# Performance work log

Hardware: AMD Instinct MI355X
Metric: run time of the kernel (lower is better)

## Reference

```python
import jax, jax.numpy as jnp
import numpy as np

NUM_ITER = 20
EPS = 1e-8


def _conv(x, w, pad):
    # x: [N, Cin, H, W], w: [Cout, Cin, kh, kw] (cross-correlation, like torch conv2d)
    return jax.lax.conv_general_dilated(
        x, w, window_strides=(1, 1), padding=pad,
        dimension_numbers=('NCHW', 'OIHW', 'NCHW'))


def setup_inputs() -> dict:
    key = jax.random.key(0)
    x = jax.random.normal(key, (2, 4, 3, 256, 256), dtype=jnp.float32)
    return {
        'x': x,
        'lam': jnp.array([0.02], dtype=jnp.float32),
        'tau': jnp.array([0.25], dtype=jnp.float32),
        'theta': jnp.array([0.1], dtype=jnp.float32),
        'wx': jnp.array([[-1.0, 1.0, 0.0]], dtype=jnp.float32),
        'wy': jnp.array([[-1.0], [1.0], [0.0]], dtype=jnp.float32),
    }


def reference(x, lam, tau, theta, wx, wy):
    # x: [2, B, C, H, W] -> pairs of single-channel images [NB, 2, H, W]
    F, B, C, H, W = x.shape
    NB = B * C
    xx = jnp.moveaxis(x.reshape(2, NB, H, W), 0, 1)  # [NB, 2, H, W]

    dt = x.dtype
    gx = jnp.array([[-1., 0., 1.], [-2., 0., 2.], [-1., 0., 1.]], dt) / 6.0
    gy = jnp.array([[-1., -2., -1.], [0., 0., 0.], [1., 2., 1.]], dt) / 6.0
    grad_w = jnp.stack([gx, gy])[:, None]          # [2,1,3,3] image gradient (fixed)
    gxu = jnp.array([[0., 0., 0.], [0., -1., 1.], [0., 0., 0.]], dt)
    gyu = jnp.array([[0., 0., 0.], [0., -1., 0.], [0., 1., 0.]], dt)
    grad_u_w = jnp.stack([gxu, gyu])[:, None]      # [2,1,3,3] flow gradient (fixed)
    wx_k = wx[None, None]                          # [1,1,1,3] trainable divergence stencil
    wy_k = wy[None, None]                          # [1,1,3,1]

    rho_c = (xx[:, 1] - xx[:, 0])[:, None]                       # [NB,1,H,W]
    grad_im = _conv(xx[:, 1:], grad_w, [(1, 1), (1, 1)])         # [NB,2,H,W]
    norm_grad = jnp.sum(grad_im * grad_im, axis=1, keepdims=True) + EPS

    u = jnp.zeros((NB, 2, H, W), dt)
    p1 = jnp.zeros((NB, 2, H, W), dt)
    p2 = jnp.zeros((NB, 2, H, W), dt)

    tl = theta * lam       # [1]
    tt = tau / theta       # [1]

    def div(p):  # p: [NB,2,H,W] -> [NB,1,H,W]
        return (_conv(p[:, 0:1], wx_k, [(0, 0), (1, 1)]) +
                _conv(p[:, 1:2], wy_k, [(1, 1), (0, 0)]))

    def body(carry, _):
        u, p1, p2 = carry
        rho = rho_c + jnp.sum(grad_im * u, axis=1, keepdims=True)
        th = tl * norm_grad
        v = u - jnp.where(jnp.abs(rho) < th,
                          rho * grad_im / norm_grad,
                          tl * grad_im * jnp.sign(rho))
        u0 = v[:, 0] + theta * div(p1)[:, 0]
        u1 = v[:, 1] + theta * div(p2)[:, 0]
        u = jnp.stack([u0, u1], axis=1)
        g1 = _conv(u[:, 0:1], grad_u_w, [(1, 1), (1, 1)])
        g2 = _conv(u[:, 1:2], grad_u_w, [(1, 1), (1, 1)])
        p1 = (p1 + tt * g1) / (1.0 + tt * jnp.sum(jnp.abs(g1), axis=1, keepdims=True))
        p2 = (p2 + tt * g2) / (1.0 + tt * jnp.sum(jnp.abs(g2), axis=1, keepdims=True))
        return (u, p1, p2), None

    (u, p1, p2), _ = jax.lax.scan(body, (u, p1, p2), None, length=NUM_ITER)
    return u.reshape(B, C, 2, H, W)
```

## Files before the change

kernel.cpp:

```cpp
#include <hip/hip_runtime.h>

#define W 256
#define H 256
#define HW (W*H)
#define NB 12
#define ROWS 16
#define BPI (H/ROWS)
#define NBLK (NB*BPI)
#define NTHREADS 1024
#define NUM_ITER 20
#define TVEPS 1e-8f
#define HPLANES 8
#define FLAG_MAGIC 0x5A170000


__device__ __forceinline__ float aload(const float* p) {
    return __hip_atomic_load(p, __ATOMIC_RELAXED, __HIP_MEMORY_SCOPE_AGENT);
}
__device__ __forceinline__ void astore(float* p, float v) {
    __hip_atomic_store(p, v, __ATOMIC_RELAXED, __HIP_MEMORY_SCOPE_AGENT);
}
__device__ __forceinline__ void waitflag(const int* f, int tgt) {
    while (__hip_atomic_load(f, __ATOMIC_RELAXED, __HIP_MEMORY_SCOPE_AGENT) != tgt)
        __builtin_amdgcn_s_sleep(1);
    asm volatile("" ::: "memory");
}
__device__ __forceinline__ void setflag(int* f, int tgt) {
    asm volatile("s_waitcnt vmcnt(0)" ::: "memory");
    __hip_atomic_store(f, tgt, __ATOMIC_RELAXED, __HIP_MEMORY_SCOPE_AGENT);
}

#define LD4(dst, ptr) { const float4 _t = *reinterpret_cast<const float4*>(ptr); \
                        dst[0]=_t.x; dst[1]=_t.y; dst[2]=_t.z; dst[3]=_t.w; }
#define ST4(ptr, src) { float4 _t; _t.x=src[0]; _t.y=src[1]; _t.z=src[2]; _t.w=src[3]; \
                        *reinterpret_cast<float4*>(ptr) = _t; }

__global__ __launch_bounds__(NTHREADS, 1) void tvl1_wave_kernel(
    const float* __restrict__ xin,
    const float* __restrict__ lam,
    const float* __restrict__ tau,
    const float* __restrict__ theta,
    const float* __restrict__ wxv,
    const float* __restrict__ wyv,
    float* __restrict__ uout,
    float* __restrict__ halo,
    int* __restrict__ flags)
{
    __shared__ float xu0[ROWS+1][W];
    __shared__ float xu1[ROWS+1][W];
    __shared__ float xq1[ROWS][W];
    __shared__ float xq2[ROWS][W];
    __shared__ float s_g16[3][W];

    const int tid  = threadIdx.x;
    const int lane = tid & 63;
    const int wv   = tid >> 6;
    const int x0   = lane << 2;
    const int b    = blockIdx.x;
    const int n    = b / BPI, bi = b % BPI;
    const int r0   = bi * ROWS;
    const int grow = r0 + wv;
    const bool notTop = (bi > 0), notBot = (bi < BPI-1);

    const float th0 = theta[0];
    const float tl  = th0 * lam[0];
    const float tt  = tau[0] / th0;
    const float wx0 = wxv[0], wx1 = wxv[1], wx2 = wxv[2];
    const float wy0 = wyv[0], wy1 = wyv[1], wy2 = wyv[2];

    const float* __restrict__ I0 = xin + (size_t)n * HW;
    const float* __restrict__ I1 = xin + (size_t)(NB + n) * HW;

    float rho[4], gxr[4], gyr[4];
    auto grad4 = [&](int row, float* rr, float* ggx, float* ggy) {
        #pragma unroll
        for (int c = 0; c < 4; ++c) {
            const int xc = x0 + c;
            const int idx = row * W + xc;
            const bool xm = xc > 0, xp = xc < W-1, ym = row > 0, yp = row < H-1;
            float a00=0.f,a01=0.f,a02=0.f,a10=0.f,a12=0.f,a20=0.f,a21=0.f,a22=0.f;
            if (ym) { a01=I1[idx-W]; if (xm) a00=I1[idx-W-1]; if (xp) a02=I1[idx-W+1]; }
            if (xm) a10=I1[idx-1];
            if (xp) a12=I1[idx+1];
            if (yp) { a21=I1[idx+W]; if (xm) a20=I1[idx+W-1]; if (xp) a22=I1[idx+W+1]; }
            ggx[c] = ((a02-a00) + 2.f*(a12-a10) + (a22-a20)) * (1.f/6.f);
            ggy[c] = ((a20-a00) + 2.f*(a21-a01) + (a22-a02)) * (1.f/6.f);
            rr[c]  = I1[idx] - I0[idx];
        }
    };
    grad4(grow, rho, gxr, gyr);
    if (wv == 14 && notBot) {
        float r2[4], g2x[4], g2y[4];
        grad4(r0 + ROWS, r2, g2x, g2y);
        ST4(&s_g16[0][x0], r2); ST4(&s_g16[1][x0], g2x); ST4(&s_g16[2][x0], g2y);
    }

    for (int k = tid; k < (ROWS+1)*W; k += NTHREADS) { (&xu0[0][0])[k]=0.f; (&xu1[0][0])[k]=0.f; }
    for (int k = tid; k < ROWS*W;     k += NTHREADS) { (&xq1[0][0])[k]=0.f; (&xq2[0][0])[k]=0.f; }
    float u0[4]={0,0,0,0}, u1[4]={0,0,0,0};
    float p1x[4]={0,0,0,0}, p1y[4]={0,0,0,0}, p2x[4]={0,0,0,0}, p2y[4]={0,0,0,0};
    __syncthreads();

    auto ustep4 = [&](const float* rr, const float* ggx, const float* ggy,
                      const float* uu0, const float* uu1,
                      const float* x1m, const float* x1c, const float* x1p,
                      const float* q1m, const float* q1c, const float* q1p,
                      const float* x2m, const float* x2c, const float* x2p,
                      const float* q2m, const float* q2c, const float* q2p,
                      float* o0, float* o1) {
        #pragma unroll
        for (int c = 0; c < 4; ++c) {
            const float r  = rr[c] + ggx[c]*uu0[c] + ggy[c]*uu1[c];
            const float ng = ggx[c]*ggx[c] + ggy[c]*ggy[c] + TVEPS;
            const float th = tl * ng;
            const float sg = (r > 0.f) ? 1.f : ((r < 0.f) ? -1.f : 0.f);
            const float f  = (fabsf(r) < th) ? (r / ng) : (tl * sg);
            const float d1 = wx0*x1m[c] + wx1*x1c[c] + wx2*x1p[c]
                           + wy0*q1m[c] + wy1*q1c[c] + wy2*q1p[c];
            const float d2 = wx0*x2m[c] + wx1*x2c[c] + wx2*x2p[c]
                           + wy0*q2m[c] + wy1*q2c[c] + wy2*q2p[c];
            o0[c] = (uu0[c] - f*ggx[c]) + th0*d1;
            o1[c] = (uu1[c] - f*ggy[c]) + th0*d2;
        }
    };

    for (int it = 0; it < NUM_ITER; ++it) {
        const bool last = (it == NUM_ITER-1);

        float hym1[4]={0,0,0,0}, hym2[4]={0,0,0,0};
        float hyp1[4]={0,0,0,0}, hyp2[4]={0,0,0,0};
        float c16x1[4]={0,0,0,0}, c16x2[4]={0,0,0,0};
        float c16c1[4]={0,0,0,0}, c16c2[4]={0,0,0,0};
        float c16p1[4]={0,0,0,0}, c16p2[4]={0,0,0,0};

        if (it > 0) {
            const float* hb = halo + (size_t)(it-1) * NBLK * HPLANES * W;
            int* fb = flags + (size_t)(it-1) * 3 * NBLK;
            const int tgt = FLAG_MAGIC | (it-1);
            if (wv == 0 && notTop) {
                if (lane == 0) waitflag(&fb[2*NBLK + (b-1)], tgt);
                const float* hu = hb + (size_t)(b-1) * HPLANES * W;
                #pragma unroll
                for (int c = 0; c < 4; ++c) {
                    hym1[c] = aload(hu + 6*W + x0 + c);
                    hym2[c] = aload(hu + 7*W + x0 + c);
                }
            }
            if (wv == 15 && notBot) {
                if (lane == 0) waitflag(&fb[0*NBLK + (b+1)], tgt);
                const float* hd = hb + (size_t)(b+1) * HPLANES * W;
                #pragma unroll
                for (int c = 0; c < 4; ++c) {
                    hyp1[c] = aload(hd + 1*W + x0 + c);
                    hyp2[c] = aload(hd + 3*W + x0 + c);
                }
            }
            if (wv == 14 && notBot && !last) {
                if (lane < 2) waitflag(&fb[lane*NBLK + (b+1)], tgt);
                const float* hd = hb + (size_t)(b+1) * HPLANES * W;
                #pragma unroll
                for (int c = 0; c < 4; ++c) {
                    c16x1[c] = aload(hd + 0*W + x0 + c);
                    c16c1[c] = aload(hd + 1*W + x0 + c);
                    c16x2[c] = aload(hd + 2*W + x0 + c);
                    c16c2[c] = aload(hd + 3*W + x0 + c);
                    c16p1[c] = aload(hd + 4*W + x0 + c);
                    c16p2[c] = aload(hd + 5*W + x0 + c);
                }
            }
        }

        float pym1[4], pym2[4], pyp1[4], pyp2[4];
        if (wv > 0) { LD4(pym1, &xq1[wv-1][x0]); LD4(pym2, &xq2[wv-1][x0]); }
        else        { for (int c=0;c<4;++c){ pym1[c]=hym1[c]; pym2[c]=hym2[c]; } }
        if (wv < ROWS-1) { LD4(pyp1, &xq1[wv+1][x0]); LD4(pyp2, &xq2[wv+1][x0]); }
        else             { for (int c=0;c<4;++c){ pyp1[c]=hyp1[c]; pyp2[c]=hyp2[c]; } }

        float l1 = __shfl_up(p1x[3], 1);   float l2 = __shfl_up(p2x[3], 1);
        if (lane == 0) { l1 = 0.f; l2 = 0.f; }
        float r1 = __shfl_down(p1x[0], 1); float r2 = __shfl_down(p2x[0], 1);
        if (lane == 63) { r1 = 0.f; r2 = 0.f; }
        const float p1xm[4] = { l1, p1x[0], p1x[1], p1x[2] };
        const float p1xp[4] = { p1x[1], p1x[2], p1x[3], r1 };
        const float p2xm[4] = { l2, p2x[0], p2x[1], p2x[2] };
        const float p2xp[4] = { p2x[1], p2x[2], p2x[3], r2 };

        float nu0[4], nu1[4];
        ustep4(rho, gxr, gyr, u0, u1,
               p1xm, p1x, p1xp, pym1, p1y, pyp1,
               p2xm, p2x, p2xp, pym2, p2y, pyp2, nu0, nu1);
        #pragma unroll
        for (int c = 0; c < 4; ++c) { u0[c] = nu0[c]; u1[c] = nu1[c]; }

        if (last) {
            float* __restrict__ o0 = uout + (size_t)(2*n)   * HW + (size_t)grow * W + x0;
            float* __restrict__ o1 = uout + (size_t)(2*n+1) * HW + (size_t)grow * W + x0;
            ST4(o0, u0); ST4(o1, u1);
            break;
        }

        ST4(&xu0[wv][x0], u0); ST4(&xu1[wv][x0], u1);

        if (wv == 14 && notBot) {
            float g16r[4], g16x[4], g16y[4], q115[4], q215[4], u160[4], u161[4];
            LD4(g16r, &s_g16[0][x0]); LD4(g16x, &s_g16[1][x0]); LD4(g16y, &s_g16[2][x0]);
            LD4(q115, &xq1[ROWS-1][x0]); LD4(q215, &xq2[ROWS-1][x0]);
            LD4(u160, &xu0[ROWS][x0]);   LD4(u161, &xu1[ROWS][x0]);
            float hl1 = __shfl_up(c16x1[3], 1), hl2 = __shfl_up(c16x2[3], 1);
            if (lane == 0) { hl1 = 0.f; hl2 = 0.f; }
            float hr1 = __shfl_down(c16x1[0], 1), hr2 = __shfl_down(c16x2[0], 1);
            if (lane == 63) { hr1 = 0.f; hr2 = 0.f; }
            const float h1m[4] = { hl1, c16x1[0], c16x1[1], c16x1[2] };
            const float h1p[4] = { c16x1[1], c16x1[2], c16x1[3], hr1 };
            const float h2m[4] = { hl2, c16x2[0], c16x2[1], c16x2[2] };
            const float h2p[4] = { c16x2[1], c16x2[2], c16x2[3], hr2 };
            float n160[4], n161[4];
            ustep4(g16r, g16x, g16y, u160, u161,
                   h1m, c16x1, h1p, q115, c16c1, c16p1,
                   h2m, c16x2, h2p, q215, c16c2, c16p2, n160, n161);
            ST4(&xu0[ROWS][x0], n160); ST4(&xu1[ROWS][x0], n161);
        }
        __syncthreads();

        float uy0[4], uy1[4];
        const bool lastRow = (grow == H-1);
        if (!lastRow) { LD4(uy0, &xu0[wv+1][x0]); LD4(uy1, &xu1[wv+1][x0]); }
        else          { for (int c=0;c<4;++c){ uy0[c]=0.f; uy1[c]=0.f; } }
        float ur0 = __shfl_down(u0[0], 1), ur1 = __shfl_down(u1[0], 1);
        if (lane == 63) { ur0 = 0.f; ur1 = 0.f; }
        #pragma unroll
        for (int c = 0; c < 4; ++c) {
            const float uxp0 = (c < 3) ? u0[c+1] : ur0;
            const float uxp1 = (c < 3) ? u1[c+1] : ur1;
            const float g1x = uxp0 - u0[c];
            const float g1y = uy0[c] - u0[c];
            const float g2x = uxp1 - u1[c];
            const float g2y = uy1[c] - u1[c];
            const float den1 = 1.f + tt * (fabsf(g1x) + fabsf(g1y));
            const float den2 = 1.f + tt * (fabsf(g2x) + fabsf(g2y));
            p1x[c] = (p1x[c] + tt*g1x) / den1;
            p1y[c] = (p1y[c] + tt*g1y) / den1;
            p2x[c] = (p2x[c] + tt*g2x) / den2;
            p2y[c] = (p2y[c] + tt*g2y) / den2;
        }
        ST4(&xq1[wv][x0], p1y); ST4(&xq2[wv][x0], p2y);

        float* hwp = halo + ((size_t)it * NBLK + b) * HPLANES * W;
        int* fw = flags + (size_t)it * 3 * NBLK;
        const int ftgt = FLAG_MAGIC | it;
        if (wv == 0) {
            #pragma unroll
            for (int c = 0; c < 4; ++c) {
                astore(hwp + 0*W + x0 + c, p1x[c]);
                astore(hwp + 1*W + x0 + c, p1y[c]);
                astore(hwp + 2*W + x0 + c, p2x[c]);
                astore(hwp + 3*W + x0 + c, p2y[c]);
            }
            if (lane == 0) setflag(&fw[0*NBLK + b], ftgt);
        } else if (wv == 1) {
            #pragma unroll
            for (int c = 0; c < 4; ++c) {
                astore(hwp + 4*W + x0 + c, p1y[c]);
                astore(hwp + 5*W + x0 + c, p2y[c]);
            }
            if (lane == 0) setflag(&fw[1*NBLK + b], ftgt);
        } else if (wv == ROWS-1) {
            #pragma unroll
            for (int c = 0; c < 4; ++c) {
                astore(hwp + 6*W + x0 + c, p1y[c]);
                astore(hwp + 7*W + x0 + c, p2y[c]);
            }
            if (lane == 0) setflag(&fw[2*NBLK + b], ftgt);
        }
        __syncthreads();
    }
}


__global__ void precompute_kernel(const float* __restrict__ x,
                                  float* __restrict__ u,
                                  float* __restrict__ ws) {
    const int row = blockIdx.x;
    const int n = row / H, y = row % H;
    const int xx = threadIdx.x;
    const int idx = y * W + xx;
    const float* __restrict__ I0 = x + (size_t)n * HW;
    const float* __restrict__ I1 = x + (size_t)(NB + n) * HW;
    float* __restrict__ p1  = ws;
    float* __restrict__ p2  = ws + (size_t)2 * NB * HW;
    float* __restrict__ rho = ws + (size_t)4 * NB * HW;
    float* __restrict__ gxp = ws + (size_t)5 * NB * HW;
    float* __restrict__ gyp = ws + (size_t)6 * NB * HW;
    const float i1c = I1[idx];
    const bool xm = xx > 0, xp = xx < W - 1, ym = y > 0, yp = y < H - 1;
    float a00=0.f,a01=0.f,a02=0.f,a10=0.f,a12=0.f,a20=0.f,a21=0.f,a22=0.f;
    if (ym) { a01 = I1[idx-W]; if (xm) a00 = I1[idx-W-1]; if (xp) a02 = I1[idx-W+1]; }
    if (xm) a10 = I1[idx-1];
    if (xp) a12 = I1[idx+1];
    if (yp) { a21 = I1[idx+W]; if (xm) a20 = I1[idx+W-1]; if (xp) a22 = I1[idx+W+1]; }
    const float gxv = ((a02-a00) + 2.f*(a12-a10) + (a22-a20)) * (1.f/6.f);
    const float gyv = ((a20-a00) + 2.f*(a21-a01) + (a22-a02)) * (1.f/6.f);
    const size_t np = (size_t)n * HW;
    rho[np+idx] = i1c - I0[idx];
    gxp[np+idx] = gxv;
    gyp[np+idx] = gyv;
    u[(size_t)(2*n)*HW + idx] = 0.f;   u[(size_t)(2*n+1)*HW + idx] = 0.f;
    p1[(size_t)(2*n)*HW + idx] = 0.f;  p1[(size_t)(2*n+1)*HW + idx] = 0.f;
    p2[(size_t)(2*n)*HW + idx] = 0.f;  p2[(size_t)(2*n+1)*HW + idx] = 0.f;
}

__global__ void u_kernel(const float* __restrict__ ws,
                         float* __restrict__ u,
                         const float* __restrict__ lam,
                         const float* __restrict__ theta,
                         const float* __restrict__ wxv,
                         const float* __restrict__ wyv) {
    const int row = blockIdx.x;
    const int n = row / H, y = row % H;
    const int xx = threadIdx.x;
    const int idx = y * W + xx;
    const size_t np = (size_t)n * HW;
    const float* __restrict__ p1  = ws;
    const float* __restrict__ p2  = ws + (size_t)2 * NB * HW;
    const float* __restrict__ rho_c = ws + (size_t)4 * NB * HW;
    const float* __restrict__ gxp = ws + (size_t)5 * NB * HW;
    const float* __restrict__ gyp = ws + (size_t)6 * NB * HW;
    const float th0 = theta[0];
    const float tl = th0 * lam[0];
    const float wx0 = wxv[0], wx1 = wxv[1], wx2 = wxv[2];
    const float wy0 = wyv[0], wy1 = wyv[1], wy2 = wyv[2];
    const float gx = gxp[np+idx];
    const float gy = gyp[np+idx];
    float* __restrict__ u0p = u + (size_t)(2*n)*HW;
    float* __restrict__ u1p = u + (size_t)(2*n+1)*HW;
    const float u0 = u0p[idx], u1 = u1p[idx];
    const float rho = rho_c[np+idx] + gx*u0 + gy*u1;
    const float ng = gx*gx + gy*gy + TVEPS;
    const float th = tl * ng;
    float s0, s1;
    if (fabsf(rho) < th) { const float d = rho/ng; s0 = d*gx; s1 = d*gy; }
    else { const float sg = (rho > 0.f) ? 1.f : ((rho < 0.f) ? -1.f : 0.f);
           s0 = tl*gx*sg; s1 = tl*gy*sg; }
    const float v0 = u0 - s0, v1 = u1 - s1;
    const float* __restrict__ p1x = p1 + (size_t)(2*n)*HW;
    const float* __restrict__ p1y = p1 + (size_t)(2*n+1)*HW;
    const float* __restrict__ p2x = p2 + (size_t)(2*n)*HW;
    const float* __restrict__ p2y = p2 + (size_t)(2*n+1)*HW;
    float d1 = wx1*p1x[idx] + wy1*p1y[idx];
    float d2 = wx1*p2x[idx] + wy1*p2y[idx];
    if (xx > 0)     { d1 += wx0*p1x[idx-1]; d2 += wx0*p2x[idx-1]; }
    if (xx < W-1)   { d1 += wx2*p1x[idx+1]; d2 += wx2*p2x[idx+1]; }
    if (y > 0)      { d1 += wy0*p1y[idx-W]; d2 += wy0*p2y[idx-W]; }
    if (y < H-1)    { d1 += wy2*p1y[idx+W]; d2 += wy2*p2y[idx+W]; }
    u0p[idx] = v0 + th0*d1;
    u1p[idx] = v1 + th0*d2;
}

__global__ void p_kernel(const float* __restrict__ u,
                         float* __restrict__ ws,
                         const float* __restrict__ tau,
                         const float* __restrict__ theta) {
    const int row = blockIdx.x;
    const int n = row / H, y = row % H;
    const int xx = threadIdx.x;
    const int idx = y * W + xx;
    float* __restrict__ p1 = ws;
    float* __restrict__ p2 = ws + (size_t)2 * NB * HW;
    const float tt = tau[0] / theta[0];
    const float* __restrict__ u0p = u + (size_t)(2*n)*HW;
    const float* __restrict__ u1p = u + (size_t)(2*n+1)*HW;
    const float c0 = u0p[idx];
    const float g1x = ((xx < W-1) ? u0p[idx+1] : 0.f) - c0;
    const float g1y = ((y < H-1) ? u0p[idx+W] : 0.f) - c0;
    const float c1 = u1p[idx];
    const float g2x = ((xx < W-1) ? u1p[idx+1] : 0.f) - c1;
    const float g2y = ((y < H-1) ? u1p[idx+W] : 0.f) - c1;
    float* __restrict__ p1x = p1 + (size_t)(2*n)*HW;
    float* __restrict__ p1y = p1 + (size_t)(2*n+1)*HW;
    float* __restrict__ p2x = p2 + (size_t)(2*n)*HW;
    float* __restrict__ p2y = p2 + (size_t)(2*n+1)*HW;
    const float den1 = 1.f + tt * (fabsf(g1x) + fabsf(g1y));
    p1x[idx] = (p1x[idx] + tt*g1x) / den1;
    p1y[idx] = (p1y[idx] + tt*g1y) / den1;
    const float den2 = 1.f + tt * (fabsf(g2x) + fabsf(g2y));
    p2x[idx] = (p2x[idx] + tt*g2x) / den2;
    p2y[idx] = (p2y[idx] + tt*g2y) / den2;
}

extern "C" void kernel_launch(void* const* d_in, const int* in_sizes, int n_in,
                              void* d_out, int out_size, void* d_ws, size_t ws_size,
                              hipStream_t stream) {
    const float* x     = (const float*)d_in[0];
    const float* lam   = (const float*)d_in[1];
    const float* tau   = (const float*)d_in[2];
    const float* theta = (const float*)d_in[3];
    const float* wxv   = (const float*)d_in[4];
    const float* wyv   = (const float*)d_in[5];
    float* u = (float*)d_out;

    const size_t halo_floats = (size_t)(NUM_ITER-1) * NBLK * HPLANES * W;
    const size_t need = halo_floats * sizeof(float)
                      + (size_t)(NUM_ITER-1) * 3 * NBLK * sizeof(int);

    if (ws_size >= need) {
        float* halo = (float*)d_ws;
        int* flags = (int*)((char*)d_ws + halo_floats * sizeof(float));
        void* args[] = { (void*)&x, (void*)&lam, (void*)&tau, (void*)&theta,
                         (void*)&wxv, (void*)&wyv, (void*)&u, (void*)&halo, (void*)&flags };
        hipLaunchCooperativeKernel((void*)tvl1_wave_kernel, dim3(NBLK), dim3(NTHREADS),
                                   args, 0, stream);
    } else {
        float* ws = (float*)d_ws;
        const dim3 grid(NB * H);
        const dim3 block(W);
        precompute_kernel<<<grid, block, 0, stream>>>(x, u, ws);
        for (int it = 0; it < NUM_ITER; ++it) {
            u_kernel<<<grid, block, 0, stream>>>(ws, u, lam, theta, wxv, wyv);
            p_kernel<<<grid, block, 0, stream>>>(u, ws, tau, theta);
        }
    }
}
```

Measured before the change: 126.8 us.

## Exchange boundary u row via halo instead of redundant row-16 recompute

Replaces the redundant recomputation of the next block's first u row, which needed six halo planes of p state, with a mid-iteration exchange: each block publishes its top u row and the bottom wave waits on the neighbour's flag before the p step. The halo shrinks from 8 to 6 planes, and extra shared-memory rows and setup work are dropped. Divisions are also replaced with hardware reciprocal approximations. The cost is an extra inter-block dependency wait inside each iteration, which can add latency on the critical path, and approximate reciprocals slightly change numerics.

```diff
diff --git a/kernel.cpp b/kernel.cpp
--- a/kernel.cpp
+++ b/kernel.cpp
@@ -10,7 +10,7 @@
 #define NTHREADS 1024
 #define NUM_ITER 20
 #define TVEPS 1e-8f
-#define HPLANES 8
+#define HPLANES 6
 #define FLAG_MAGIC 0x5A170000
 
 
@@ -29,13 +29,14 @@
     asm volatile("s_waitcnt vmcnt(0)" ::: "memory");
     __hip_atomic_store(f, tgt, __ATOMIC_RELAXED, __HIP_MEMORY_SCOPE_AGENT);
 }
+__device__ __forceinline__ float fastrcp(float x) { return __builtin_amdgcn_rcpf(x); }
 
 #define LD4(dst, ptr) { const float4 _t = *reinterpret_cast<const float4*>(ptr); \
                         dst[0]=_t.x; dst[1]=_t.y; dst[2]=_t.z; dst[3]=_t.w; }
 #define ST4(ptr, src) { float4 _t; _t.x=src[0]; _t.y=src[1]; _t.z=src[2]; _t.w=src[3]; \
                         *reinterpret_cast<float4*>(ptr) = _t; }
 
-__global__ __launch_bounds__(NTHREADS, 1) void tvl1_wave_kernel(
+__global__ __launch_bounds__(NTHREADS, 1) void tvl1_uex_kernel(
     const float* __restrict__ xin,
     const float* __restrict__ lam,
     const float* __restrict__ tau,
@@ -46,11 +47,10 @@
     float* __restrict__ halo,
     int* __restrict__ flags)
 {
-    __shared__ float xu0[ROWS+1][W];
-    __shared__ float xu1[ROWS+1][W];
+    __shared__ float xu0[ROWS][W];
+    __shared__ float xu1[ROWS][W];
     __shared__ float xq1[ROWS][W];
     __shared__ float xq2[ROWS][W];
-    __shared__ float s_g16[3][W];
 
     const int tid  = threadIdx.x;
     const int lane = tid & 63;
@@ -72,100 +72,55 @@
     const float* __restrict__ I1 = xin + (size_t)(NB + n) * HW;
 
     float rho[4], gxr[4], gyr[4];
-    auto grad4 = [&](int row, float* rr, float* ggx, float* ggy) {
+    {
         #pragma unroll
         for (int c = 0; c < 4; ++c) {
             const int xc = x0 + c;
-            const int idx = row * W + xc;
-            const bool xm = xc > 0, xp = xc < W-1, ym = row > 0, yp = row < H-1;
+            const int idx = grow * W + xc;
+            const bool xm = xc > 0, xp = xc < W-1, ym = grow > 0, yp = grow < H-1;
             float a00=0.f,a01=0.f,a02=0.f,a10=0.f,a12=0.f,a20=0.f,a21=0.f,a22=0.f;
             if (ym) { a01=I1[idx-W]; if (xm) a00=I1[idx-W-1]; if (xp) a02=I1[idx-W+1]; }
             if (xm) a10=I1[idx-1];
             if (xp) a12=I1[idx+1];
             if (yp) { a21=I1[idx+W]; if (xm) a20=I1[idx+W-1]; if (xp) a22=I1[idx+W+1]; }
-            ggx[c] = ((a02-a00) + 2.f*(a12-a10) + (a22-a20)) * (1.f/6.f);
-            ggy[c] = ((a20-a00) + 2.f*(a21-a01) + (a22-a02)) * (1.f/6.f);
-            rr[c]  = I1[idx] - I0[idx];
-        }
-    };
-    grad4(grow, rho, gxr, gyr);
-    if (wv == 14 && notBot) {
-        float r2[4], g2x[4], g2y[4];
-        grad4(r0 + ROWS, r2, g2x, g2y);
-        ST4(&s_g16[0][x0], r2); ST4(&s_g16[1][x0], g2x); ST4(&s_g16[2][x0], g2y);
+            gxr[c] = ((a02-a00) + 2.f*(a12-a10) + (a22-a20)) * (1.f/6.f);
+            gyr[c] = ((a20-a00) + 2.f*(a21-a01) + (a22-a02)) * (1.f/6.f);
+            rho[c] = I1[idx] - I0[idx];
+        }
     }
 
-    for (int k = tid; k < (ROWS+1)*W; k += NTHREADS) { (&xu0[0][0])[k]=0.f; (&xu1[0][0])[k]=0.f; }
-    for (int k = tid; k < ROWS*W;     k += NTHREADS) { (&xq1[0][0])[k]=0.f; (&xq2[0][0])[k]=0.f; }
+    for (int k = tid; k < ROWS*W; k += NTHREADS) {
+        (&xu0[0][0])[k]=0.f; (&xu1[0][0])[k]=0.f;
+        (&xq1[0][0])[k]=0.f; (&xq2[0][0])[k]=0.f;
+    }
     float u0[4]={0,0,0,0}, u1[4]={0,0,0,0};
     float p1x[4]={0,0,0,0}, p1y[4]={0,0,0,0}, p2x[4]={0,0,0,0}, p2y[4]={0,0,0,0};
     __syncthreads();
 
-    auto ustep4 = [&](const float* rr, const float* ggx, const float* ggy,
-                      const float* uu0, const float* uu1,
-                      const float* x1m, const float* x1c, const float* x1p,
-                      const float* q1m, const float* q1c, const float* q1p,
-                      const float* x2m, const float* x2c, const float* x2p,
-                      const float* q2m, const float* q2c, const float* q2p,
-                      float* o0, float* o1) {
-        #pragma unroll
-        for (int c = 0; c < 4; ++c) {
-            const float r  = rr[c] + ggx[c]*uu0[c] + ggy[c]*uu1[c];
-            const float ng = ggx[c]*ggx[c] + ggy[c]*ggy[c] + TVEPS;
-            const float th = tl * ng;
-            const float sg = (r > 0.f) ? 1.f : ((r < 0.f) ? -1.f : 0.f);
-            const float f  = (fabsf(r) < th) ? (r / ng) : (tl * sg);
-            const float d1 = wx0*x1m[c] + wx1*x1c[c] + wx2*x1p[c]
-                           + wy0*q1m[c] + wy1*q1c[c] + wy2*q1p[c];
-            const float d2 = wx0*x2m[c] + wx1*x2c[c] + wx2*x2p[c]
-                           + wy0*q2m[c] + wy1*q2c[c] + wy2*q2p[c];
-            o0[c] = (uu0[c] - f*ggx[c]) + th0*d1;
-            o1[c] = (uu1[c] - f*ggy[c]) + th0*d2;
-        }
-    };
-
     for (int it = 0; it < NUM_ITER; ++it) {
         const bool last = (it == NUM_ITER-1);
 
         float hym1[4]={0,0,0,0}, hym2[4]={0,0,0,0};
         float hyp1[4]={0,0,0,0}, hyp2[4]={0,0,0,0};
-        float c16x1[4]={0,0,0,0}, c16x2[4]={0,0,0,0};
-        float c16c1[4]={0,0,0,0}, c16c2[4]={0,0,0,0};
-        float c16p1[4]={0,0,0,0}, c16p2[4]={0,0,0,0};
-
         if (it > 0) {
-            const float* hb = halo + (size_t)(it-1) * NBLK * HPLANES * W;
             int* fb = flags + (size_t)(it-1) * 3 * NBLK;
             const int tgt = FLAG_MAGIC | (it-1);
             if (wv == 0 && notTop) {
-                if (lane == 0) waitflag(&fb[2*NBLK + (b-1)], tgt);
-                const float* hu = hb + (size_t)(b-1) * HPLANES * W;
+                if (lane == 0) waitflag(&fb[1*NBLK + (b-1)], tgt);
+                const float* hu = halo + ((size_t)(it-1)*NBLK + (b-1)) * HPLANES * W;
                 #pragma unroll
                 for (int c = 0; c < 4; ++c) {
-                    hym1[c] = aload(hu + 6*W + x0 + c);
-                    hym2[c] = aload(hu + 7*W + x0 + c);
+                    hym1[c] = aload(hu + 2*W + x0 + c);
+                    hym2[c] = aload(hu + 3*W + x0 + c);
                 }
             }
             if (wv == 15 && notBot) {
                 if (lane == 0) waitflag(&fb[0*NBLK + (b+1)], tgt);
-                const float* hd = hb + (size_t)(b+1) * HPLANES * W;
+                const float* hd = halo + ((size_t)(it-1)*NBLK + (b+1)) * HPLANES * W;
                 #pragma unroll
                 for (int c = 0; c < 4; ++c) {
-                    hyp1[c] = aload(hd + 1*W + x0 + c);
-                    hyp2[c] = aload(hd + 3*W + x0 + c);
-                }
-            }
-            if (wv == 14 && notBot && !last) {
-                if (lane < 2) waitflag(&fb[lane*NBLK + (b+1)], tgt);
-                const float* hd = hb + (size_t)(b+1) * HPLANES * W;
-                #pragma unroll
-                for (int c = 0; c < 4; ++c) {
-                    c16x1[c] = aload(hd + 0*W + x0 + c);
-                    c16c1[c] = aload(hd + 1*W + x0 + c);
-                    c16x2[c] = aload(hd + 2*W + x0 + c);
-                    c16c2[c] = aload(hd + 3*W + x0 + c);
-                    c16p1[c] = aload(hd + 4*W + x0 + c);
-                    c16p2[c] = aload(hd + 5*W + x0 + c);
+                    hyp1[c] = aload(hd + 0*W + x0 + c);
+                    hyp2[c] = aload(hd + 1*W + x0 + c);
                 }
             }
         }
@@ -185,12 +140,19 @@
         const float p2xm[4] = { l2, p2x[0], p2x[1], p2x[2] };
         const float p2xp[4] = { p2x[1], p2x[2], p2x[3], r2 };
 
-        float nu0[4], nu1[4];
-        ustep4(rho, gxr, gyr, u0, u1,
-               p1xm, p1x, p1xp, pym1, p1y, pyp1,
-               p2xm, p2x, p2xp, pym2, p2y, pyp2, nu0, nu1);
         #pragma unroll
-        for (int c = 0; c < 4; ++c) { u0[c] = nu0[c]; u1[c] = nu1[c]; }
+        for (int c = 0; c < 4; ++c) {
+            const float r  = rho[c] + gxr[c]*u0[c] + gyr[c]*u1[c];
+            const float ng = gxr[c]*gxr[c] + gyr[c]*gyr[c] + TVEPS;
+            const float th = tl * ng;
+            const float f  = (fabsf(r) < th) ? (r * fastrcp(ng)) : copysignf(tl, r);
+            const float d1 = wx0*p1xm[c] + wx1*p1x[c] + wx2*p1xp[c]
+                           + wy0*pym1[c] + wy1*p1y[c] + wy2*pyp1[c];
+            const float d2 = wx0*p2xm[c] + wx1*p2x[c] + wx2*p2xp[c]
+                           + wy0*pym2[c] + wy1*p2y[c] + wy2*pyp2[c];
+            u0[c] = (u0[c] - f*gxr[c]) + th0*d1;
+            u1[c] = (u1[c] - f*gyr[c]) + th0*d2;
+        }
 
         if (last) {
             float* __restrict__ o0 = uout + (size_t)(2*n)   * HW + (size_t)grow * W + x0;
@@ -199,33 +161,32 @@
             break;
         }
 
+        float* hwp = halo + ((size_t)it * NBLK + b) * HPLANES * W;
+        int* fw = flags + (size_t)it * 3 * NBLK;
+        const int ftgt = FLAG_MAGIC | it;
+        if (wv == 0 && notTop) {
+            #pragma unroll
+            for (int c = 0; c < 4; ++c) {
+                astore(hwp + 4*W + x0 + c, u0[c]);
+                astore(hwp + 5*W + x0 + c, u1[c]);
+            }
+            if (lane == 0) setflag(&fw[2*NBLK + b], ftgt);
+        }
         ST4(&xu0[wv][x0], u0); ST4(&xu1[wv][x0], u1);
-
-        if (wv == 14 && notBot) {
-            float g16r[4], g16x[4], g16y[4], q115[4], q215[4], u160[4], u161[4];
-            LD4(g16r, &s_g16[0][x0]); LD4(g16x, &s_g16[1][x0]); LD4(g16y, &s_g16[2][x0]);
-            LD4(q115, &xq1[ROWS-1][x0]); LD4(q215, &xq2[ROWS-1][x0]);
-            LD4(u160, &xu0[ROWS][x0]);   LD4(u161, &xu1[ROWS][x0]);
-            float hl1 = __shfl_up(c16x1[3], 1), hl2 = __shfl_up(c16x2[3], 1);
-            if (lane == 0) { hl1 = 0.f; hl2 = 0.f; }
-            float hr1 = __shfl_down(c16x1[0], 1), hr2 = __shfl_down(c16x2[0], 1);
-            if (lane == 63) { hr1 = 0.f; hr2 = 0.f; }
-            const float h1m[4] = { hl1, c16x1[0], c16x1[1], c16x1[2] };
-            const float h1p[4] = { c16x1[1], c16x1[2], c16x1[3], hr1 };
-            const float h2m[4] = { hl2, c16x2[0], c16x2[1], c16x2[2] };
-            const float h2p[4] = { c16x2[1], c16x2[2], c16x2[3], hr2 };
-            float n160[4], n161[4];
-            ustep4(g16r, g16x, g16y, u160, u161,
-                   h1m, c16x1, h1p, q115, c16c1, c16p1,
-                   h2m, c16x2, h2p, q215, c16c2, c16p2, n160, n161);
-            ST4(&xu0[ROWS][x0], n160); ST4(&xu1[ROWS][x0], n161);
-        }
         __syncthreads();
 
         float uy0[4], uy1[4];
-        const bool lastRow = (grow == H-1);
-        if (!lastRow) { LD4(uy0, &xu0[wv+1][x0]); LD4(uy1, &xu1[wv+1][x0]); }
-        else          { for (int c=0;c<4;++c){ uy0[c]=0.f; uy1[c]=0.f; } }
+        if (wv < ROWS-1) { LD4(uy0, &xu0[wv+1][x0]); LD4(uy1, &xu1[wv+1][x0]); }
+        else if (grow == H-1) { for (int c=0;c<4;++c){ uy0[c]=0.f; uy1[c]=0.f; } }
+        else {
+            if (lane == 0) waitflag(&fw[2*NBLK + (b+1)], ftgt);
+            const float* hd = halo + ((size_t)it*NBLK + (b+1)) * HPLANES * W;
+            #pragma unroll
+            for (int c = 0; c < 4; ++c) {
+                uy0[c] = aload(hd + 4*W + x0 + c);
+                uy1[c] = aload(hd + 5*W + x0 + c);
+            }
+        }
         float ur0 = __shfl_down(u0[0], 1), ur1 = __shfl_down(u1[0], 1);
         if (lane == 63) { ur0 = 0.f; ur1 = 0.f; }
         #pragma unroll
@@ -236,41 +197,29 @@
             const float g1y = uy0[c] - u0[c];
             const float g2x = uxp1 - u1[c];
             const float g2y = uy1[c] - u1[c];
-            const float den1 = 1.f + tt * (fabsf(g1x) + fabsf(g1y));
-            const float den2 = 1.f + tt * (fabsf(g2x) + fabsf(g2y));
-            p1x[c] = (p1x[c] + tt*g1x) / den1;
-            p1y[c] = (p1y[c] + tt*g1y) / den1;
-            p2x[c] = (p2x[c] + tt*g2x) / den2;
-            p2y[c] = (p2y[c] + tt*g2y) / den2;
+            const float rc1 = fastrcp(1.f + tt * (fabsf(g1x) + fabsf(g1y)));
+            const float rc2 = fastrcp(1.f + tt * (fabsf(g2x) + fabsf(g2y)));
+            p1x[c] = (p1x[c] + tt*g1x) * rc1;
+            p1y[c] = (p1y[c] + tt*g1y) * rc1;
+            p2x[c] = (p2x[c] + tt*g2x) * rc2;
+            p2y[c] = (p2y[c] + tt*g2y) * rc2;
         }
         ST4(&xq1[wv][x0], p1y); ST4(&xq2[wv][x0], p2y);
 
-        float* hwp = halo + ((size_t)it * NBLK + b) * HPLANES * W;
-        int* fw = flags + (size_t)it * 3 * NBLK;
-        const int ftgt = FLAG_MAGIC | it;
-        if (wv == 0) {
+        if (wv == 0 && notTop) {
             #pragma unroll
             for (int c = 0; c < 4; ++c) {
-                astore(hwp + 0*W + x0 + c, p1x[c]);
-                astore(hwp + 1*W + x0 + c, p1y[c]);
-                astore(hwp + 2*W + x0 + c, p2x[c]);
-                astore(hwp + 3*W + x0 + c, p2y[c]);
+                astore(hwp + 0*W + x0 + c, p1y[c]);
+                astore(hwp + 1*W + x0 + c, p2y[c]);
             }
             if (lane == 0) setflag(&fw[0*NBLK + b], ftgt);
-        } else if (wv == 1) {
+        } else if (wv == ROWS-1 && notBot) {
             #pragma unroll
             for (int c = 0; c < 4; ++c) {
-                astore(hwp + 4*W + x0 + c, p1y[c]);
-                astore(hwp + 5*W + x0 + c, p2y[c]);
+                astore(hwp + 2*W + x0 + c, p1y[c]);
+                astore(hwp + 3*W + x0 + c, p2y[c]);
             }
             if (lane == 0) setflag(&fw[1*NBLK + b], ftgt);
-        } else if (wv == ROWS-1) {
-            #pragma unroll
-            for (int c = 0; c < 4; ++c) {
-                astore(hwp + 6*W + x0 + c, p1y[c]);
-                astore(hwp + 7*W + x0 + c, p2y[c]);
-            }
-            if (lane == 0) setflag(&fw[2*NBLK + b], ftgt);
         }
         __syncthreads();
     }
@@ -407,7 +356,7 @@
         int* flags = (int*)((char*)d_ws + halo_floats * sizeof(float));
         void* args[] = { (void*)&x, (void*)&lam, (void*)&tau, (void*)&theta,
                          (void*)&wxv, (void*)&wyv, (void*)&u, (void*)&halo, (void*)&flags };
-        hipLaunchCooperativeKernel((void*)tvl1_wave_kernel, dim3(NBLK), dim3(NTHREADS),
+        hipLaunchCooperativeKernel((void*)tvl1_uex_kernel, dim3(NBLK), dim3(NTHREADS),
                                    args, 0, stream);
     } else {
         float* ws = (float*)d_ws;
```

Measured after the change: 102.4 us. 1.24x faster.
